# Kernel optimization log

Hardware: AMD Instinct MI355X
Metric: run time of the kernel (lower is better)

Reference implementation:

```python
import jax, jax.numpy as jnp
import numpy as np

N_NODES = 100000
N_EDGES = 1600000
C_IN, C_HID, C_OUT = 64, 64, 32


def _gcn_conv(x, src, dst, ew, W, b, n_nodes):
    """PyG GCNConv: add self-loops (weight 1), symmetric normalization,
    out[dst] += norm * (x @ W)[src], plus bias. Dropout omitted (eval mode)."""
    h = x @ W  # [N, C_out_layer]
    loop = jnp.arange(n_nodes, dtype=src.dtype)
    src_a = jnp.concatenate([src, loop])
    dst_a = jnp.concatenate([dst, loop])
    ew_a = jnp.concatenate([ew, jnp.ones((n_nodes,), dtype=ew.dtype)])
    # degree over incoming (dst) side, weighted
    deg = jax.ops.segment_sum(ew_a, dst_a, num_segments=n_nodes)
    dinv = jnp.where(deg > 0, jax.lax.rsqrt(deg), 0.0)
    norm = dinv[src_a] * ew_a * dinv[dst_a]  # [E+N]
    msg = h[src_a] * norm[:, None]           # gather + scale: [E+N, C]
    out = jax.ops.segment_sum(msg, dst_a, num_segments=n_nodes)  # scatter-add
    return out + b


def setup_inputs() -> dict:
    key = jax.random.key(0)
    k1, k2, k3, k4, k5, k6, k7 = jax.random.split(key, 7)
    x = jax.random.normal(k1, (N_NODES, C_IN), dtype=jnp.float32)
    edge_index = jax.random.randint(k2, (2, N_EDGES), 0, N_NODES, dtype=jnp.int64)
    edge_attr = jax.random.uniform(k3, (N_EDGES,), dtype=jnp.float32)
    s1 = 1.0 / np.sqrt(C_IN)
    s2 = 1.0 / np.sqrt(C_HID)
    W1 = jax.random.uniform(k4, (C_IN, C_HID), jnp.float32, -s1, s1)
    b1 = jnp.zeros((C_HID,), dtype=jnp.float32)
    W2 = jax.random.uniform(k5, (C_HID, C_OUT), jnp.float32, -s2, s2)
    b2 = jnp.zeros((C_OUT,), dtype=jnp.float32)
    return {"x": x, "edge_index": edge_index, "edge_attr": edge_attr,
            "W1": W1, "b1": b1, "W2": W2, "b2": b2}


def reference(x, edge_index, edge_attr, W1, b1, W2, b2):
    n = x.shape[0]
    src, dst = edge_index[0], edge_index[1]
    h = _gcn_conv(x, src, dst, edge_attr, W1, b1, n)
    h = jax.nn.relu(h)  # dropout is identity in eval mode
    out = _gcn_conv(h, src, dst, edge_attr, W2, b2, n)
    return out
```

## Files before the change

kernel.cpp:

```cpp
#include <hip/hip_runtime.h>
#include <hip/hip_fp16.h>


#define TPB 256
#define TPB_P 512
#define TPB_S 1024
#define BSH2 8
#define BN2 256
#define NBC 512
#define PCHUNK 4096
#define CAP2 5632
#define XSTR 68

typedef union { uint2 u; __half2 h[2]; } hpack;
typedef union { uint4 u; __half2 h[4]; } hpack8;

__device__ __forceinline__ int enc_w(float w) {
  unsigned b = __float_as_uint(w);
  return (int)(((b + 0x7FFFu + ((b >> 16) & 1u)) >> 16) & 0x7FFFu);
}
__device__ __forceinline__ float dec_w(int e) {
  return __uint_as_float(((unsigned)e >> 17) << 16);
}

__global__ __launch_bounds__(TPB_P) void k_part(const int* __restrict__ si,
                                                const int* __restrict__ di,
                                                const float* __restrict__ ew,
                                                int* __restrict__ bpos,
                                                int2* __restrict__ tin, int e) {
  __shared__ int hcnt[NBC];
  __shared__ int lst0[NBC];
  __shared__ int lcur[NBC];
  __shared__ int hbase[NBC];
  __shared__ int2 se[PCHUNK];
  __shared__ unsigned short sbk[PCHUNK];
  int t = threadIdx.x;
  int lo = blockIdx.x * PCHUNK;
  int hi = lo + PCHUNK; if (hi > e) hi = e;
  int cn = hi - lo;
  hcnt[t] = 0;
  __syncthreads();
  for (int i = lo + t; i < hi; i += TPB_P) atomicAdd(&hcnt[di[i] >> BSH2], 1);
  __syncthreads();
  int c = hcnt[t];
  for (int off = 1; off < NBC; off <<= 1) {
    int u = (t >= off) ? hcnt[t - off] : 0;
    __syncthreads();
    hcnt[t] += u;
    __syncthreads();
  }
  {
    int ex = hcnt[t] - c;
    lst0[t] = ex;
    lcur[t] = 0;
    hbase[t] = c ? (t * CAP2 + atomicAdd(&bpos[t], c)) : 0;
  }
  __syncthreads();
  for (int i = lo + t; i < hi; i += TPB_P) {
    int d = di[i];
    int bk = d >> BSH2;
    int loc = atomicAdd(&lcur[bk], 1);
    int p = lst0[bk] + loc;
    se[p] = make_int2(si[i] | ((d & (BN2 - 1)) << 17), __float_as_int(ew[i]));
    sbk[p] = (unsigned short)bk;
  }
  __syncthreads();
  for (int p = t; p < cn; p += TPB_P) {
    int bk = sbk[p];
    tin[hbase[bk] + (p - lst0[bk])] = se[p];
  }
}

__global__ __launch_bounds__(TPB_S) void k_sortb(const int2* __restrict__ tin,
                                                 const int* __restrict__ bpos,
                                                 int* __restrict__ colpk,
                                                 int2* __restrict__ rowseg,
                                                 float* __restrict__ dinv, int n) {
  __shared__ int cnt[BN2];
  __shared__ float degw[BN2];
  __shared__ int cur[BN2];
  __shared__ int ls[BN2];
  int b = blockIdx.x, t = threadIdx.x;
  if (t < BN2) { cnt[t] = 0; degw[t] = 1.0f; }
  __syncthreads();
  int jb = b * CAP2, je = jb + bpos[b];
  for (int j = jb + t; j < je; j += TPB_S) {
    int2 p = tin[j];
    int dl = p.x >> 17;
    atomicAdd(&cnt[dl], 1);
    atomicAdd(&degw[dl], __int_as_float(p.y));
  }
  __syncthreads();
  int c = (t < BN2) ? cnt[t] : 0;
  int c4 = (c + 3) & ~3;
  if (t < BN2) ls[t] = c4;
  __syncthreads();
  for (int off = 1; off < BN2; off <<= 1) {
    int u = (t >= off && t < BN2) ? ls[t - off] : 0;
    __syncthreads();
    if (t < BN2) ls[t] += u;
    __syncthreads();
  }
  int base = b << BSH2;
  if (t < BN2) {
    int start = jb + ls[t] - c4;
    cur[t] = start;
    int node = base + t;
    if (node < n) {
      rowseg[node] = make_int2(start, start + c4);
      dinv[node] = rsqrtf(degw[t]);
    }
    for (int i = c; i < c4; ++i) colpk[start + i] = 0;
  }
  __syncthreads();
  for (int j = jb + t; j < je; j += TPB_S) {
    int2 p = tin[j];
    int dl = p.x >> 17;
    int pos = atomicAdd(&cur[dl], 1);
    colpk[pos] = (p.x & 0x1FFFF) | (enc_w(__int_as_float(p.y)) << 17);
  }
}

__global__ __launch_bounds__(TPB) void k_gemm1(const float* __restrict__ x,
                                               const float* __restrict__ W1,
                                               const float* __restrict__ dinv,
                                               __half* __restrict__ g1h, int n) {
  __shared__ float Wl[64 * 64];
  int t = threadIdx.x;
  {
    const float4* W4 = (const float4*)W1;
    float4* Wl4 = (float4*)Wl;
#pragma unroll
    for (int i = 0; i < 4; ++i) Wl4[t + TPB * i] = W4[t + TPB * i];
  }
  __syncthreads();
  int r = blockIdx.x * 16 + (t >> 4);
  if (r >= n) return;
  int c0 = (t & 15) << 2;
  const float4* xr = (const float4*)(x + (size_t)r * 64);
  float ax = 0.f, ay = 0.f, az = 0.f, aw = 0.f;
#pragma unroll
  for (int kk = 0; kk < 16; ++kk) {
    float4 xv = xr[kk];
    const float* w = &Wl[(kk * 4) * 64 + c0];
    float4 w0 = *(const float4*)(w);
    float4 w1 = *(const float4*)(w + 64);
    float4 w2 = *(const float4*)(w + 128);
    float4 w3 = *(const float4*)(w + 192);
    ax += xv.x * w0.x + xv.y * w1.x + xv.z * w2.x + xv.w * w3.x;
    ay += xv.x * w0.y + xv.y * w1.y + xv.z * w2.y + xv.w * w3.y;
    az += xv.x * w0.z + xv.y * w1.z + xv.z * w2.z + xv.w * w3.z;
    aw += xv.x * w0.w + xv.y * w1.w + xv.z * w2.w + xv.w * w3.w;
  }
  float dv = dinv[r];
  hpack pk;
  pk.h[0] = __floats2half2_rn(dv * ax, dv * ay);
  pk.h[1] = __floats2half2_rn(dv * az, dv * aw);
  *(uint2*)(g1h + (size_t)r * 64 + c0) = pk.u;
}

__global__ __launch_bounds__(TPB) void k_gfuse(const __half* __restrict__ g1h,
                                               const int* __restrict__ colpk,
                                               const int2* __restrict__ rowseg,
                                               const float* __restrict__ dinv,
                                               const float* __restrict__ W2,
                                               const float* __restrict__ b1,
                                               __half* __restrict__ g2h, int n) {
  __shared__ float W2l[64 * 32];
  __shared__ float b1l[64];
  __shared__ float x2l[32 * XSTR];
  int t = threadIdx.x;
  {
    const float4* W4 = (const float4*)W2;
    float4* Wl4 = (float4*)W2l;
#pragma unroll
    for (int i = 0; i < 2; ++i) Wl4[t + TPB * i] = W4[t + TPB * i];
    if (t < 64) b1l[t] = b1[t];
  }
  __syncthreads();
  int node = t >> 3;
  int r = blockIdx.x * 32 + node;
  int c0 = (t & 7) << 3;
  bool valid = (r < n);
  float a[8];
  float dv = 0.f;
  if (valid) {
    dv = dinv[r];
    hpack8 s; s.u = *(const uint4*)(g1h + (size_t)r * 64 + c0);
#pragma unroll
    for (int k = 0; k < 4; ++k) {
      float2 f = __half22float2(s.h[k]);
      a[2 * k] = f.x; a[2 * k + 1] = f.y;
    }
    int2 seg = rowseg[r];
    int j = seg.x;
    for (; j + 7 < seg.y; j += 8) {
      int4 qa = *(const int4*)(colpk + j);
      int4 qb = *(const int4*)(colpk + j + 4);
      hpack8 u0; u0.u = *(const uint4*)(g1h + (size_t)(qa.x & 0x1FFFF) * 64 + c0);
      hpack8 u1; u1.u = *(const uint4*)(g1h + (size_t)(qa.y & 0x1FFFF) * 64 + c0);
      hpack8 u2; u2.u = *(const uint4*)(g1h + (size_t)(qa.z & 0x1FFFF) * 64 + c0);
      hpack8 u3; u3.u = *(const uint4*)(g1h + (size_t)(qa.w & 0x1FFFF) * 64 + c0);
      hpack8 u4; u4.u = *(const uint4*)(g1h + (size_t)(qb.x & 0x1FFFF) * 64 + c0);
      hpack8 u5; u5.u = *(const uint4*)(g1h + (size_t)(qb.y & 0x1FFFF) * 64 + c0);
      hpack8 u6; u6.u = *(const uint4*)(g1h + (size_t)(qb.z & 0x1FFFF) * 64 + c0);
      hpack8 u7; u7.u = *(const uint4*)(g1h + (size_t)(qb.w & 0x1FFFF) * 64 + c0);
      float w0 = dec_w(qa.x), w1 = dec_w(qa.y), w2 = dec_w(qa.z), w3 = dec_w(qa.w);
      float w4 = dec_w(qb.x), w5 = dec_w(qb.y), w6 = dec_w(qb.z), w7 = dec_w(qb.w);
#pragma unroll
      for (int k = 0; k < 4; ++k) {
        float2 f;
        f = __half22float2(u0.h[k]); a[2*k] += w0 * f.x; a[2*k+1] += w0 * f.y;
        f = __half22float2(u1.h[k]); a[2*k] += w1 * f.x; a[2*k+1] += w1 * f.y;
        f = __half22float2(u2.h[k]); a[2*k] += w2 * f.x; a[2*k+1] += w2 * f.y;
        f = __half22float2(u3.h[k]); a[2*k] += w3 * f.x; a[2*k+1] += w3 * f.y;
        f = __half22float2(u4.h[k]); a[2*k] += w4 * f.x; a[2*k+1] += w4 * f.y;
        f = __half22float2(u5.h[k]); a[2*k] += w5 * f.x; a[2*k+1] += w5 * f.y;
        f = __half22float2(u6.h[k]); a[2*k] += w6 * f.x; a[2*k+1] += w6 * f.y;
        f = __half22float2(u7.h[k]); a[2*k] += w7 * f.x; a[2*k+1] += w7 * f.y;
      }
    }
    if (j < seg.y) {
      int4 qa = *(const int4*)(colpk + j);
      hpack8 u0; u0.u = *(const uint4*)(g1h + (size_t)(qa.x & 0x1FFFF) * 64 + c0);
      hpack8 u1; u1.u = *(const uint4*)(g1h + (size_t)(qa.y & 0x1FFFF) * 64 + c0);
      hpack8 u2; u2.u = *(const uint4*)(g1h + (size_t)(qa.z & 0x1FFFF) * 64 + c0);
      hpack8 u3; u3.u = *(const uint4*)(g1h + (size_t)(qa.w & 0x1FFFF) * 64 + c0);
      float w0 = dec_w(qa.x), w1 = dec_w(qa.y), w2 = dec_w(qa.z), w3 = dec_w(qa.w);
#pragma unroll
      for (int k = 0; k < 4; ++k) {
        float2 f;
        f = __half22float2(u0.h[k]); a[2*k] += w0 * f.x; a[2*k+1] += w0 * f.y;
        f = __half22float2(u1.h[k]); a[2*k] += w1 * f.x; a[2*k+1] += w1 * f.y;
        f = __half22float2(u2.h[k]); a[2*k] += w2 * f.x; a[2*k+1] += w2 * f.y;
        f = __half22float2(u3.h[k]); a[2*k] += w3 * f.x; a[2*k+1] += w3 * f.y;
      }
    }
    float* xp = x2l + node * XSTR + c0;
#pragma unroll
    for (int k = 0; k < 8; k += 4) {
      float4 v = {fmaxf(dv * a[k + 0] + b1l[c0 + k + 0], 0.f),
                  fmaxf(dv * a[k + 1] + b1l[c0 + k + 1], 0.f),
                  fmaxf(dv * a[k + 2] + b1l[c0 + k + 2], 0.f),
                  fmaxf(dv * a[k + 3] + b1l[c0 + k + 3], 0.f)};
      *(float4*)(xp + k) = v;
    }
  }
  __syncthreads();
  if (!valid) return;
  int oc = (t & 7) << 2;
  const float* xr = x2l + node * XSTR;
  float ax = 0.f, ay = 0.f, az = 0.f, aw = 0.f;
#pragma unroll
  for (int kk = 0; kk < 16; ++kk) {
    float4 xv = *(const float4*)(xr + 4 * kk);
    const float* w = &W2l[(kk * 4) * 32 + oc];
    float4 w0 = *(const float4*)(w);
    float4 w1 = *(const float4*)(w + 32);
    float4 w2 = *(const float4*)(w + 64);
    float4 w3 = *(const float4*)(w + 96);
    ax += xv.x * w0.x + xv.y * w1.x + xv.z * w2.x + xv.w * w3.x;
    ay += xv.x * w0.y + xv.y * w1.y + xv.z * w2.y + xv.w * w3.y;
    az += xv.x * w0.z + xv.y * w1.z + xv.z * w2.z + xv.w * w3.z;
    aw += xv.x * w0.w + xv.y * w1.w + xv.z * w2.w + xv.w * w3.w;
  }
  hpack pk;
  pk.h[0] = __floats2half2_rn(dv * ax, dv * ay);
  pk.h[1] = __floats2half2_rn(dv * az, dv * aw);
  *(uint2*)(g2h + (size_t)r * 32 + oc) = pk.u;
}

__global__ __launch_bounds__(TPB) void k_gather32(const __half* __restrict__ g2h,
                                                  const int* __restrict__ colpk,
                                                  const int2* __restrict__ rowseg,
                                                  const float* __restrict__ dinv,
                                                  const float* __restrict__ b2,
                                                  float* __restrict__ out, int n) {
  int t = threadIdx.x;
  int r = blockIdx.x * 64 + (t >> 2);
  if (r >= n) return;
  int c0 = (t & 3) << 3;
  float a[8];
  {
    hpack8 s; s.u = *(const uint4*)(g2h + (size_t)r * 32 + c0);
#pragma unroll
    for (int k = 0; k < 4; ++k) {
      float2 f = __half22float2(s.h[k]);
      a[2 * k] = f.x; a[2 * k + 1] = f.y;
    }
  }
  int2 seg = rowseg[r];
  int j = seg.x;
  for (; j + 7 < seg.y; j += 8) {
    int4 qa = *(const int4*)(colpk + j);
    int4 qb = *(const int4*)(colpk + j + 4);
    hpack8 u0; u0.u = *(const uint4*)(g2h + (size_t)(qa.x & 0x1FFFF) * 32 + c0);
    hpack8 u1; u1.u = *(const uint4*)(g2h + (size_t)(qa.y & 0x1FFFF) * 32 + c0);
    hpack8 u2; u2.u = *(const uint4*)(g2h + (size_t)(qa.z & 0x1FFFF) * 32 + c0);
    hpack8 u3; u3.u = *(const uint4*)(g2h + (size_t)(qa.w & 0x1FFFF) * 32 + c0);
    hpack8 u4; u4.u = *(const uint4*)(g2h + (size_t)(qb.x & 0x1FFFF) * 32 + c0);
    hpack8 u5; u5.u = *(const uint4*)(g2h + (size_t)(qb.y & 0x1FFFF) * 32 + c0);
    hpack8 u6; u6.u = *(const uint4*)(g2h + (size_t)(qb.z & 0x1FFFF) * 32 + c0);
    hpack8 u7; u7.u = *(const uint4*)(g2h + (size_t)(qb.w & 0x1FFFF) * 32 + c0);
    float w0 = dec_w(qa.x), w1 = dec_w(qa.y), w2 = dec_w(qa.z), w3 = dec_w(qa.w);
    float w4 = dec_w(qb.x), w5 = dec_w(qb.y), w6 = dec_w(qb.z), w7 = dec_w(qb.w);
#pragma unroll
    for (int k = 0; k < 4; ++k) {
      float2 f;
      f = __half22float2(u0.h[k]); a[2*k] += w0 * f.x; a[2*k+1] += w0 * f.y;
      f = __half22float2(u1.h[k]); a[2*k] += w1 * f.x; a[2*k+1] += w1 * f.y;
      f = __half22float2(u2.h[k]); a[2*k] += w2 * f.x; a[2*k+1] += w2 * f.y;
      f = __half22float2(u3.h[k]); a[2*k] += w3 * f.x; a[2*k+1] += w3 * f.y;
      f = __half22float2(u4.h[k]); a[2*k] += w4 * f.x; a[2*k+1] += w4 * f.y;
      f = __half22float2(u5.h[k]); a[2*k] += w5 * f.x; a[2*k+1] += w5 * f.y;
      f = __half22float2(u6.h[k]); a[2*k] += w6 * f.x; a[2*k+1] += w6 * f.y;
      f = __half22float2(u7.h[k]); a[2*k] += w7 * f.x; a[2*k+1] += w7 * f.y;
    }
  }
  if (j < seg.y) {
    int4 qa = *(const int4*)(colpk + j);
    hpack8 u0; u0.u = *(const uint4*)(g2h + (size_t)(qa.x & 0x1FFFF) * 32 + c0);
    hpack8 u1; u1.u = *(const uint4*)(g2h + (size_t)(qa.y & 0x1FFFF) * 32 + c0);
    hpack8 u2; u2.u = *(const uint4*)(g2h + (size_t)(qa.z & 0x1FFFF) * 32 + c0);
    hpack8 u3; u3.u = *(const uint4*)(g2h + (size_t)(qa.w & 0x1FFFF) * 32 + c0);
    float w0 = dec_w(qa.x), w1 = dec_w(qa.y), w2 = dec_w(qa.z), w3 = dec_w(qa.w);
#pragma unroll
    for (int k = 0; k < 4; ++k) {
      float2 f;
      f = __half22float2(u0.h[k]); a[2*k] += w0 * f.x; a[2*k+1] += w0 * f.y;
      f = __half22float2(u1.h[k]); a[2*k] += w1 * f.x; a[2*k+1] += w1 * f.y;
      f = __half22float2(u2.h[k]); a[2*k] += w2 * f.x; a[2*k+1] += w2 * f.y;
      f = __half22float2(u3.h[k]); a[2*k] += w3 * f.x; a[2*k+1] += w3 * f.y;
    }
  }
  float dv = dinv[r];
  const float4* b24 = (const float4*)(b2 + c0);
  float4 bb0 = b24[0], bb1 = b24[1];
  float* op = out + (size_t)r * 32 + c0;
  *(float4*)(op)     = make_float4(dv * a[0] + bb0.x, dv * a[1] + bb0.y,
                                   dv * a[2] + bb0.z, dv * a[3] + bb0.w);
  *(float4*)(op + 4) = make_float4(dv * a[4] + bb1.x, dv * a[5] + bb1.y,
                                   dv * a[6] + bb1.z, dv * a[7] + bb1.w);
}

extern "C" void kernel_launch(void* const* d_in, const int* in_sizes, int n_in,
                              void* d_out, int out_size, void* d_ws, size_t ws_size,
                              hipStream_t stream) {
  const float* x  = (const float*)d_in[0];
  const int* ei   = (const int*)d_in[1];
  const float* ew = (const float*)d_in[2];
  const float* W1 = (const float*)d_in[3];
  const float* b1 = (const float*)d_in[4];
  const float* W2 = (const float*)d_in[5];
  const float* b2 = (const float*)d_in[6];
  float* out = (float*)d_out;

  const int n = in_sizes[0] / 64;
  const int e = in_sizes[1] / 2;
  const int* si = ei;
  const int* di = ei + e;
  const int NBc = (n + BN2 - 1) >> BSH2;

  float* ws = (float*)d_ws;
  const size_t NP = 100352;
  const size_t SLOTS = (size_t)NBc * CAP2;
  float*  dinv   = ws;
  __half* g1h    = (__half*)(ws + NP);
  int2*   rowseg = (int2*)(ws + NP + (size_t)n * 32);
  int*    bpos   = (int*)(rowseg + NP);
  int*    colpk  = bpos + 1024;
  int2*   tin    = (int2*)(colpk + SLOTS);
  __half* g2h    = (__half*)(tin + SLOTS);

  int gb_part = (e + PCHUNK - 1) / PCHUNK;
  int gb_g1 = (n + 15) / 16;
  int gb_gf = (n + 31) / 32;
  int gb_g32 = (n + 63) / 64;

  hipMemsetAsync(bpos, 0, NBC * sizeof(int), stream);
  k_part<<<gb_part, TPB_P, 0, stream>>>(si, di, ew, bpos, tin, e);
  k_sortb<<<NBc, TPB_S, 0, stream>>>(tin, bpos, colpk, rowseg, dinv, n);
  k_gemm1<<<gb_g1, TPB, 0, stream>>>(x, W1, dinv, g1h, n);
  k_gfuse<<<gb_gf, TPB, 0, stream>>>(g1h, colpk, rowseg, dinv, W2, b1, g2h, n);
  k_gather32<<<gb_g32, TPB, 0, stream>>>(g2h, colpk, rowseg, dinv, b2, out, n);
}
```

Measured before the change: 205.4 us.

## Replace two-pass bucket partition sort with global-atomic count/scan/scatter CSR build

```diff
diff --git a/kernel.cpp b/kernel.cpp
--- a/kernel.cpp
+++ b/kernel.cpp
@@ -3,12 +3,8 @@
 
 
 #define TPB 256
-#define TPB_P 512
-#define TPB_S 1024
 #define BSH2 8
 #define BN2 256
-#define NBC 512
-#define PCHUNK 4096
 #define CAP2 5632
 #define XSTR 68
 
@@ -23,101 +19,77 @@
   return __uint_as_float(((unsigned)e >> 17) << 16);
 }
 
-__global__ __launch_bounds__(TPB_P) void k_part(const int* __restrict__ si,
-                                                const int* __restrict__ di,
-                                                const float* __restrict__ ew,
-                                                int* __restrict__ bpos,
-                                                int2* __restrict__ tin, int e) {
-  __shared__ int hcnt[NBC];
-  __shared__ int lst0[NBC];
-  __shared__ int lcur[NBC];
-  __shared__ int hbase[NBC];
-  __shared__ int2 se[PCHUNK];
-  __shared__ unsigned short sbk[PCHUNK];
-  int t = threadIdx.x;
-  int lo = blockIdx.x * PCHUNK;
-  int hi = lo + PCHUNK; if (hi > e) hi = e;
-  int cn = hi - lo;
-  hcnt[t] = 0;
-  __syncthreads();
-  for (int i = lo + t; i < hi; i += TPB_P) atomicAdd(&hcnt[di[i] >> BSH2], 1);
-  __syncthreads();
-  int c = hcnt[t];
-  for (int off = 1; off < NBC; off <<= 1) {
-    int u = (t >= off) ? hcnt[t - off] : 0;
-    __syncthreads();
-    hcnt[t] += u;
-    __syncthreads();
-  }
-  {
-    int ex = hcnt[t] - c;
-    lst0[t] = ex;
-    lcur[t] = 0;
-    hbase[t] = c ? (t * CAP2 + atomicAdd(&bpos[t], c)) : 0;
-  }
-  __syncthreads();
-  for (int i = lo + t; i < hi; i += TPB_P) {
-    int d = di[i];
-    int bk = d >> BSH2;
-    int loc = atomicAdd(&lcur[bk], 1);
-    int p = lst0[bk] + loc;
-    se[p] = make_int2(si[i] | ((d & (BN2 - 1)) << 17), __float_as_int(ew[i]));
-    sbk[p] = (unsigned short)bk;
-  }
-  __syncthreads();
-  for (int p = t; p < cn; p += TPB_P) {
-    int bk = sbk[p];
-    tin[hbase[bk] + (p - lst0[bk])] = se[p];
-  }
-}
-
-__global__ __launch_bounds__(TPB_S) void k_sortb(const int2* __restrict__ tin,
-                                                 const int* __restrict__ bpos,
-                                                 int* __restrict__ colpk,
-                                                 int2* __restrict__ rowseg,
-                                                 float* __restrict__ dinv, int n) {
-  __shared__ int cnt[BN2];
-  __shared__ float degw[BN2];
-  __shared__ int cur[BN2];
+__global__ __launch_bounds__(TPB) void k_cnt(const int* __restrict__ di,
+                                             const float* __restrict__ ew,
+                                             int* __restrict__ cnt,
+                                             float* __restrict__ degw, int e) {
+  int i4 = (blockIdx.x * TPB + threadIdx.x) << 2;
+  if (i4 + 3 < e) {
+    int4 d = *(const int4*)(di + i4);
+    float4 w = *(const float4*)(ew + i4);
+    atomicAdd(&cnt[d.x], 1); atomicAdd(&degw[d.x], w.x);
+    atomicAdd(&cnt[d.y], 1); atomicAdd(&degw[d.y], w.y);
+    atomicAdd(&cnt[d.z], 1); atomicAdd(&degw[d.z], w.z);
+    atomicAdd(&cnt[d.w], 1); atomicAdd(&degw[d.w], w.w);
+  } else {
+    for (int k = i4; k < e; ++k) {
+      atomicAdd(&cnt[di[k]], 1);
+      atomicAdd(&degw[di[k]], ew[k]);
+    }
+  }
+}
+
+__global__ __launch_bounds__(BN2) void k_scan(const int* __restrict__ cnt,
+                                              const float* __restrict__ degw,
+                                              int* __restrict__ cur,
+                                              int2* __restrict__ rowseg,
+                                              float* __restrict__ dinv,
+                                              int* __restrict__ colpk, int n) {
   __shared__ int ls[BN2];
   int b = blockIdx.x, t = threadIdx.x;
-  if (t < BN2) { cnt[t] = 0; degw[t] = 1.0f; }
-  __syncthreads();
-  int jb = b * CAP2, je = jb + bpos[b];
-  for (int j = jb + t; j < je; j += TPB_S) {
-    int2 p = tin[j];
-    int dl = p.x >> 17;
-    atomicAdd(&cnt[dl], 1);
-    atomicAdd(&degw[dl], __int_as_float(p.y));
-  }
-  __syncthreads();
-  int c = (t < BN2) ? cnt[t] : 0;
+  int node = (b << BSH2) + t;
+  int c = (node < n) ? cnt[node] : 0;
   int c4 = (c + 3) & ~3;
-  if (t < BN2) ls[t] = c4;
+  ls[t] = c4;
   __syncthreads();
   for (int off = 1; off < BN2; off <<= 1) {
-    int u = (t >= off && t < BN2) ? ls[t - off] : 0;
+    int u = (t >= off) ? ls[t - off] : 0;
     __syncthreads();
-    if (t < BN2) ls[t] += u;
+    ls[t] += u;
     __syncthreads();
   }
-  int base = b << BSH2;
-  if (t < BN2) {
-    int start = jb + ls[t] - c4;
-    cur[t] = start;
-    int node = base + t;
-    if (node < n) {
-      rowseg[node] = make_int2(start, start + c4);
-      dinv[node] = rsqrtf(degw[t]);
-    }
+  if (node < n) {
+    int start = b * CAP2 + ls[t] - c4;
+    rowseg[node] = make_int2(start, start + c4);
+    cur[node] = start;
+    dinv[node] = rsqrtf(1.0f + degw[node]);
     for (int i = c; i < c4; ++i) colpk[start + i] = 0;
   }
-  __syncthreads();
-  for (int j = jb + t; j < je; j += TPB_S) {
-    int2 p = tin[j];
-    int dl = p.x >> 17;
-    int pos = atomicAdd(&cur[dl], 1);
-    colpk[pos] = (p.x & 0x1FFFF) | (enc_w(__int_as_float(p.y)) << 17);
+}
+
+__global__ __launch_bounds__(TPB) void k_scat(const int* __restrict__ si,
+                                              const int* __restrict__ di,
+                                              const float* __restrict__ ew,
+                                              int* __restrict__ cur,
+                                              int* __restrict__ colpk, int e) {
+  int i4 = (blockIdx.x * TPB + threadIdx.x) << 2;
+  if (i4 + 3 < e) {
+    int4 s = *(const int4*)(si + i4);
+    int4 d = *(const int4*)(di + i4);
+    float4 w = *(const float4*)(ew + i4);
+    int p0 = atomicAdd(&cur[d.x], 1);
+    int p1 = atomicAdd(&cur[d.y], 1);
+    int p2 = atomicAdd(&cur[d.z], 1);
+    int p3 = atomicAdd(&cur[d.w], 1);
+    colpk[p0] = (s.x & 0x1FFFF) | (enc_w(w.x) << 17);
+    colpk[p1] = (s.y & 0x1FFFF) | (enc_w(w.y) << 17);
+    colpk[p2] = (s.z & 0x1FFFF) | (enc_w(w.z) << 17);
+    colpk[p3] = (s.w & 0x1FFFF) | (enc_w(w.w) << 17);
+  } else {
+    for (int k = i4; k < e; ++k) {
+      int p = atomicAdd(&cur[di[k]], 1);
+      colpk[p] = (si[k] & 0x1FFFF) | (enc_w(ew[k]) << 17);
+    }
   }
 }
 
@@ -367,19 +339,21 @@
   float*  dinv   = ws;
   __half* g1h    = (__half*)(ws + NP);
   int2*   rowseg = (int2*)(ws + NP + (size_t)n * 32);
-  int*    bpos   = (int*)(rowseg + NP);
-  int*    colpk  = bpos + 1024;
-  int2*   tin    = (int2*)(colpk + SLOTS);
-  __half* g2h    = (__half*)(tin + SLOTS);
-
-  int gb_part = (e + PCHUNK - 1) / PCHUNK;
+  int*    cnt    = (int*)(rowseg + NP);
+  float*  degw   = (float*)(cnt + NP);
+  int*    cur    = (int*)(degw + NP);
+  int*    colpk  = cur + NP;
+  __half* g2h    = (__half*)(colpk + SLOTS);
+
+  int gb_e4 = ((e + 3) / 4 + TPB - 1) / TPB;
   int gb_g1 = (n + 15) / 16;
   int gb_gf = (n + 31) / 32;
   int gb_g32 = (n + 63) / 64;
 
-  hipMemsetAsync(bpos, 0, NBC * sizeof(int), stream);
-  k_part<<<gb_part, TPB_P, 0, stream>>>(si, di, ew, bpos, tin, e);
-  k_sortb<<<NBc, TPB_S, 0, stream>>>(tin, bpos, colpk, rowseg, dinv, n);
+  hipMemsetAsync(cnt, 0, 2 * NP * sizeof(int), stream);
+  k_cnt<<<gb_e4, TPB, 0, stream>>>(di, ew, cnt, degw, e);
+  k_scan<<<NBc, BN2, 0, stream>>>(cnt, degw, cur, rowseg, dinv, colpk, n);
+  k_scat<<<gb_e4, TPB, 0, stream>>>(si, di, ew, cur, colpk, e);
   k_gemm1<<<gb_g1, TPB, 0, stream>>>(x, W1, dinv, g1h, n);
   k_gfuse<<<gb_gf, TPB, 0, stream>>>(g1h, colpk, rowseg, dinv, W2, b1, g2h, n);
   k_gather32<<<gb_g32, TPB, 0, stream>>>(g2h, colpk, rowseg, dinv, b2, out, n);
```

Result: slower. 422.8 us (+105.9%).
